# Performance work log

Measured on AMD Instinct MI355X. Metric: run time of the kernel, lower is better.

The kernel has to match this reference:

```python
import jax, jax.numpy as jnp
import numpy as np

N_NODES = 100_000
N_EDGES = 3_200_000
D_IN = 128
D_OUT = 128


def setup_inputs() -> dict:
    key = jax.random.key(0)
    k1, k2, k3, k4 = jax.random.split(key, 4)
    x = jax.random.normal(k1, (N_NODES, D_IN), dtype=jnp.float32)
    edge_index = jax.random.randint(k2, (2, N_EDGES), 0, N_NODES, dtype=jnp.int32)
    # nn.Linear(in, out): W is [out, in], b is [out]
    W = jax.random.normal(k3, (D_OUT, D_IN), dtype=jnp.float32) * (1.0 / np.sqrt(D_IN))
    b = jax.random.normal(k4, (D_OUT,), dtype=jnp.float32) * 0.01
    return {"x": x, "edge_index": edge_index, "W": W, "b": b}


def reference(x, edge_index, W, b):
    row, col = edge_index[0], edge_index[1]
    # deg = bincount(row); symmetric-normalization coefficients per edge
    deg = jax.ops.segment_sum(jnp.ones(row.shape[0], dtype=x.dtype), row,
                              num_segments=N_NODES)
    deg_inv_sqrt = jnp.where(deg > 0, jax.lax.rsqrt(deg), 0.0)
    norm = deg_inv_sqrt[row] * deg_inv_sqrt[col]  # [E]
    # linear transform then SpMM aggregation: out[i] = sum_{e: row[e]=i} norm[e] * xl[col[e]]
    xl = x @ W.T + b  # [N, D_OUT]
    out = jax.ops.segment_sum(norm[:, None] * xl[col], row, num_segments=N_NODES)
    return out
```

## Files before the change

### kernel.cpp

```cpp
#include <hip/hip_runtime.h>
#include <hip/hip_bf16.h>

#define N_NODES 100000
#define N_EDGES 3200000
#define D 128
#define NB 782
#define CAP 5120
#define EPB 32
#define K2 20

typedef __attribute__((ext_vector_type(8))) short short8v;
typedef __attribute__((ext_vector_type(4))) float f32x4;

static __device__ __forceinline__ short f2bf(float f) {
    __hip_bfloat16 h = __float2bfloat16(f);
    return __builtin_bit_cast(short, h);
}

__global__ __launch_bounds__(256) void partition_k(const int* __restrict__ ei,
                                                   int* __restrict__ cursor,
                                                   int* __restrict__ staging) {
    __shared__ int lbin[NB];
    int tid = threadIdx.x;
    long long base = (long long)blockIdx.x * (256 * EPB);

    for (int i = tid; i < NB; i += 256) lbin[i] = 0;
    __syncthreads();

    int lrec[EPB];
    int lpk[EPB];
#pragma unroll
    for (int j = 0; j < EPB; ++j) {
        long long e = base + j * 256 + tid;
        lpk[j] = -1;
        if (e < N_EDGES) {
            int r = ei[e];
            int c = ei[N_EDGES + e];
            int bin = r >> 7;
            int rank = atomicAdd(&lbin[bin], 1);
            lrec[j] = (c << 7) | (r & 127);
            lpk[j] = (bin << 16) | rank;
        }
    }
    __syncthreads();
    for (int i = tid; i < NB; i += 256) {
        int c = lbin[i];
        if (c > 0) lbin[i] = i * CAP + atomicAdd(&cursor[i], c);
    }
    __syncthreads();
#pragma unroll
    for (int j = 0; j < EPB; ++j) {
        if (lpk[j] >= 0) {
            int bin = ((unsigned)lpk[j]) >> 16;
            int rank = lpk[j] & 0xffff;
            staging[lbin[bin] + rank] = lrec[j];
        }
    }
}

__global__ __launch_bounds__(64) void bscan_k(const int* __restrict__ cursor,
                                              int* __restrict__ fbase) {
    int lane = threadIdx.x;
    const int CH = (NB + 63) / 64;
    int v[CH];
    int t = 0;
#pragma unroll
    for (int k = 0; k < CH; ++k) {
        int idx = lane * CH + k;
        int c = (idx < NB) ? cursor[idx] : 0;
        v[k] = t;
        t += c;
    }
    int x = t;
    for (int off = 1; off < 64; off <<= 1) {
        int y = __shfl_up(x, off, 64);
        if (lane >= off) x += y;
    }
    int excl = x - t;
#pragma unroll
    for (int k = 0; k < CH; ++k) {
        int idx = lane * CH + k;
        if (idx < NB) fbase[idx] = excl + v[k];
    }
}

__global__ __launch_bounds__(256) void pass2_k(const int* __restrict__ staging,
                                               const int* __restrict__ cursor,
                                               const int* __restrict__ fbase,
                                               int* __restrict__ rowptr,
                                               float* __restrict__ dinv,
                                               int* __restrict__ edgesF) {
    __shared__ int hist[128];
    __shared__ int ssc[128];
    int bin = blockIdx.x;
    int tid = threadIdx.x;
    int cnt = cursor[bin];
    int fb = fbase[bin];
    int row0 = bin << 7;
    const int* st = staging + bin * CAP;

    if (tid < 128) hist[tid] = 0;
    __syncthreads();

    int myrec[K2];
    int myrank[K2];
#pragma unroll
    for (int k = 0; k < K2; ++k) {
        int idx = k * 256 + tid;
        myrec[k] = (idx < cnt) ? st[idx] : -1;
    }
#pragma unroll
    for (int k = 0; k < K2; ++k) {
        myrank[k] = (myrec[k] >= 0) ? atomicAdd(&hist[myrec[k] & 127], 1) : 0;
    }
    __syncthreads();
    if (tid < 128) ssc[tid] = hist[tid];
    __syncthreads();
    for (int off = 1; off < 128; off <<= 1) {
        int t = (tid < 128 && tid >= off) ? ssc[tid - off] : 0;
        __syncthreads();
        if (tid < 128) ssc[tid] += t;
        __syncthreads();
    }
    if (tid < 128) {
        int row = row0 + tid;
        if (row < N_NODES) {
            int deg = hist[tid];
            rowptr[row] = fb + ssc[tid] - deg;
            dinv[row] = (deg > 0) ? rsqrtf((float)deg) : 0.0f;
        }
    }
    if (bin == 0 && tid == 0) rowptr[N_NODES] = N_EDGES;
    __syncthreads();
#pragma unroll
    for (int k = 0; k < K2; ++k) {
        if (myrec[k] >= 0) {
            int r = myrec[k] & 127;
            int c = ((unsigned)myrec[k]) >> 7;
            edgesF[fb + ssc[r] - hist[r] + myrank[k]] = c;
        }
    }
}

__global__ __launch_bounds__(256) void convW(const float* __restrict__ W,
                                             __hip_bfloat16* __restrict__ Wb) {
    int i = blockIdx.x * 256 + threadIdx.x;
    if (i < D * D) Wb[i] = __float2bfloat16(W[i]);
}

__global__ __launch_bounds__(256) void gemm_mfma(const float* __restrict__ x,
                                                 const __hip_bfloat16* __restrict__ Wb,
                                                 const float* __restrict__ b,
                                                 const float* __restrict__ dinv,
                                                 __hip_bfloat16* __restrict__ xl) {
    __shared__ __hip_bfloat16 lds[4][16][136];
    int tid = threadIdx.x;
    int w = tid >> 6;
    int l = tid & 63;
    int lm = l & 15;
    int kb = l >> 4;
    int bm = blockIdx.x * 64 + w * 16;

    int row = bm + lm;
    if (row >= N_NODES) row = N_NODES - 1;
    const float* xr = x + (size_t)row * D;

    short8v a[4];
#pragma unroll
    for (int ks = 0; ks < 4; ++ks) {
        const float* p = xr + ks * 32 + kb * 8;
        float4 u = *(const float4*)p;
        float4 v = *(const float4*)(p + 4);
        short8v t;
        t[0] = f2bf(u.x); t[1] = f2bf(u.y); t[2] = f2bf(u.z); t[3] = f2bf(u.w);
        t[4] = f2bf(v.x); t[5] = f2bf(v.y); t[6] = f2bf(v.z); t[7] = f2bf(v.w);
        a[ks] = t;
    }

    f32x4 acc[8];
#pragma unroll
    for (int nf = 0; nf < 8; ++nf) {
        acc[nf][0] = 0.f; acc[nf][1] = 0.f; acc[nf][2] = 0.f; acc[nf][3] = 0.f;
    }

    const short8v* Wv = reinterpret_cast<const short8v*>(Wb);
#pragma unroll
    for (int ks = 0; ks < 4; ++ks) {
#pragma unroll
        for (int nf = 0; nf < 8; ++nf) {
            short8v bf = Wv[(nf * 16 + lm) * 16 + ks * 4 + kb];
            acc[nf] = __builtin_amdgcn_mfma_f32_16x16x32_bf16(a[ks], bf, acc[nf], 0, 0, 0);
        }
    }

    float drj[4];
#pragma unroll
    for (int j = 0; j < 4; ++j) {
        int rr = bm + kb * 4 + j;
        if (rr >= N_NODES) rr = N_NODES - 1;
        drj[j] = dinv[rr];
    }

#pragma unroll
    for (int nf = 0; nf < 8; ++nf) {
        float bias = b[nf * 16 + lm];
#pragma unroll
        for (int j = 0; j < 4; ++j) {
            lds[w][kb * 4 + j][nf * 16 + lm] =
                __float2bfloat16((acc[nf][j] + bias) * drj[j]);
        }
    }
    __syncthreads();
#pragma unroll
    for (int it = 0; it < 4; ++it) {
        int idx = it * 64 + l;
        int r = idx >> 4;
        int ch = (idx & 15) * 8;
        int grow = bm + r;
        if (grow < N_NODES)
            *(short8v*)&xl[(size_t)grow * D + ch] = *(const short8v*)&lds[w][r][ch];
    }
}

__global__ __launch_bounds__(256) void aggregate(const int* __restrict__ edges,
                                                 const int* __restrict__ rowptr,
                                                 const float* __restrict__ dinv,
                                                 const __hip_bfloat16* __restrict__ xl,
                                                 float* __restrict__ out) {
    int gw = (blockIdx.x * 256 + threadIdx.x) >> 6;
    int lane = threadIdx.x & 63;
    if (gw >= N_NODES) return;
    int g = lane >> 4;
    int q = lane & 15;
    int s = rowptr[gw];
    int e = rowptr[gw + 1];

    float acc[8];
#pragma unroll
    for (int k = 0; k < 8; ++k) acc[k] = 0.0f;

    int i = s;
    for (; i + 4 <= e; i += 4) {
        int c = edges[i + g];
        uint4 v = *(const uint4*)&xl[(size_t)c * D + q * 8];
        acc[0] += __uint_as_float(v.x << 16);
        acc[1] += __uint_as_float(v.x & 0xffff0000u);
        acc[2] += __uint_as_float(v.y << 16);
        acc[3] += __uint_as_float(v.y & 0xffff0000u);
        acc[4] += __uint_as_float(v.z << 16);
        acc[5] += __uint_as_float(v.z & 0xffff0000u);
        acc[6] += __uint_as_float(v.w << 16);
        acc[7] += __uint_as_float(v.w & 0xffff0000u);
    }
    int rem = e - i;
    if (g < rem) {
        int c = edges[i + g];
        uint4 v = *(const uint4*)&xl[(size_t)c * D + q * 8];
        acc[0] += __uint_as_float(v.x << 16);
        acc[1] += __uint_as_float(v.x & 0xffff0000u);
        acc[2] += __uint_as_float(v.y << 16);
        acc[3] += __uint_as_float(v.y & 0xffff0000u);
        acc[4] += __uint_as_float(v.z << 16);
        acc[5] += __uint_as_float(v.z & 0xffff0000u);
        acc[6] += __uint_as_float(v.w << 16);
        acc[7] += __uint_as_float(v.w & 0xffff0000u);
    }
#pragma unroll
    for (int k = 0; k < 8; ++k) {
        acc[k] += __shfl_xor(acc[k], 16, 64);
        acc[k] += __shfl_xor(acc[k], 32, 64);
    }
    if (lane < 16) {
        float dr = dinv[gw];
        float4 o0 = make_float4(dr * acc[0], dr * acc[1], dr * acc[2], dr * acc[3]);
        float4 o1 = make_float4(dr * acc[4], dr * acc[5], dr * acc[6], dr * acc[7]);
        float* op = &out[(size_t)gw * D + q * 8];
        *(float4*)op = o0;
        *(float4*)(op + 4) = o1;
    }
}

extern "C" void kernel_launch(void* const* d_in, const int* in_sizes, int n_in,
                              void* d_out, int out_size, void* d_ws, size_t ws_size,
                              hipStream_t stream) {
    const float* x  = (const float*)d_in[0];
    const int*   ei = (const int*)d_in[1];
    const float* W  = (const float*)d_in[2];
    const float* b  = (const float*)d_in[3];
    float* out = (float*)d_out;

    unsigned int* ws = (unsigned int*)d_ws;
    __hip_bfloat16* xl = (__hip_bfloat16*)ws;
    __hip_bfloat16* Wb = (__hip_bfloat16*)(ws + 6400000);
    float* dinv    = (float*)(ws + 6408192);
    int*   rowptr  = (int*)(ws + 6508288);
    int*   cursor  = (int*)(ws + 6608448);
    int*   fbase   = (int*)(ws + 6609248);
    int*   edgesF  = (int*)(ws + 6610048);
    int*   staging = (int*)(ws + 9810048);

    hipMemsetAsync(cursor, 0, NB * sizeof(int), stream);

    const int pblocks = (N_EDGES + 256 * EPB - 1) / (256 * EPB);
    partition_k<<<pblocks, 256, 0, stream>>>(ei, cursor, staging);

    bscan_k<<<1, 64, 0, stream>>>(cursor, fbase);

    pass2_k<<<NB, 256, 0, stream>>>(staging, cursor, fbase, rowptr, dinv, edgesF);

    convW<<<(D * D + 255) / 256, 256, 0, stream>>>(W, Wb);

    gemm_mfma<<<(N_NODES + 63) / 64, 256, 0, stream>>>(x, Wb, b, dinv, xl);

    aggregate<<<(N_NODES * 64 + 255) / 256, 256, 0, stream>>>(
        edgesF, rowptr, dinv, xl, out);
}
```

Before: 318.8 us.

## Merge memset, W conversion and bin scan into fewer launches; unroll aggregate gather

```diff
diff --git a/kernel.cpp b/kernel.cpp
--- a/kernel.cpp
+++ b/kernel.cpp
@@ -15,6 +15,14 @@
 static __device__ __forceinline__ short f2bf(float f) {
     __hip_bfloat16 h = __float2bfloat16(f);
     return __builtin_bit_cast(short, h);
+}
+
+__global__ __launch_bounds__(256) void convW_init(const float* __restrict__ W,
+                                                  __hip_bfloat16* __restrict__ Wb,
+                                                  int* __restrict__ cursor) {
+    int i = blockIdx.x * 256 + threadIdx.x;
+    if (i < D * D) Wb[i] = __float2bfloat16(W[i]);
+    if (i < NB) cursor[i] = 0;
 }
 
 __global__ __launch_bounds__(256) void partition_k(const int* __restrict__ ei,
@@ -58,49 +66,28 @@
     }
 }
 
-__global__ __launch_bounds__(64) void bscan_k(const int* __restrict__ cursor,
-                                              int* __restrict__ fbase) {
-    int lane = threadIdx.x;
-    const int CH = (NB + 63) / 64;
-    int v[CH];
-    int t = 0;
-#pragma unroll
-    for (int k = 0; k < CH; ++k) {
-        int idx = lane * CH + k;
-        int c = (idx < NB) ? cursor[idx] : 0;
-        v[k] = t;
-        t += c;
-    }
-    int x = t;
-    for (int off = 1; off < 64; off <<= 1) {
-        int y = __shfl_up(x, off, 64);
-        if (lane >= off) x += y;
-    }
-    int excl = x - t;
-#pragma unroll
-    for (int k = 0; k < CH; ++k) {
-        int idx = lane * CH + k;
-        if (idx < NB) fbase[idx] = excl + v[k];
-    }
-}
-
 __global__ __launch_bounds__(256) void pass2_k(const int* __restrict__ staging,
                                                const int* __restrict__ cursor,
-                                               const int* __restrict__ fbase,
                                                int* __restrict__ rowptr,
                                                float* __restrict__ dinv,
                                                int* __restrict__ edgesF) {
     __shared__ int hist[128];
     __shared__ int ssc[128];
+    __shared__ int wsum[4];
     int bin = blockIdx.x;
     int tid = threadIdx.x;
     int cnt = cursor[bin];
-    int fb = fbase[bin];
     int row0 = bin << 7;
     const int* st = staging + bin * CAP;
 
+    int pacc = 0;
+    for (int j = tid; j < bin; j += 256) pacc += cursor[j];
+#pragma unroll
+    for (int off = 32; off > 0; off >>= 1) pacc += __shfl_down(pacc, off, 64);
+    if ((tid & 63) == 0) wsum[tid >> 6] = pacc;
     if (tid < 128) hist[tid] = 0;
     __syncthreads();
+    int fb = wsum[0] + wsum[1] + wsum[2] + wsum[3];
 
     int myrec[K2];
     int myrank[K2];
@@ -140,12 +127,6 @@
             edgesF[fb + ssc[r] - hist[r] + myrank[k]] = c;
         }
     }
-}
-
-__global__ __launch_bounds__(256) void convW(const float* __restrict__ W,
-                                             __hip_bfloat16* __restrict__ Wb) {
-    int i = blockIdx.x * 256 + threadIdx.x;
-    if (i < D * D) Wb[i] = __float2bfloat16(W[i]);
 }
 
 __global__ __launch_bounds__(256) void gemm_mfma(const float* __restrict__ x,
@@ -222,6 +203,17 @@
     }
 }
 
+static __device__ __forceinline__ void acc8(float* acc, uint4 v) {
+    acc[0] += __uint_as_float(v.x << 16);
+    acc[1] += __uint_as_float(v.x & 0xffff0000u);
+    acc[2] += __uint_as_float(v.y << 16);
+    acc[3] += __uint_as_float(v.y & 0xffff0000u);
+    acc[4] += __uint_as_float(v.z << 16);
+    acc[5] += __uint_as_float(v.z & 0xffff0000u);
+    acc[6] += __uint_as_float(v.w << 16);
+    acc[7] += __uint_as_float(v.w & 0xffff0000u);
+}
+
 __global__ __launch_bounds__(256) void aggregate(const int* __restrict__ edges,
                                                  const int* __restrict__ rowptr,
                                                  const float* __restrict__ dinv,
@@ -240,30 +232,27 @@
     for (int k = 0; k < 8; ++k) acc[k] = 0.0f;
 
     int i = s;
+    for (; i + 16 <= e; i += 16) {
+        int c0 = edges[i + g];
+        int c1 = edges[i + 4 + g];
+        int c2 = edges[i + 8 + g];
+        int c3 = edges[i + 12 + g];
+        uint4 v0 = *(const uint4*)&xl[(size_t)c0 * D + q * 8];
+        uint4 v1 = *(const uint4*)&xl[(size_t)c1 * D + q * 8];
+        uint4 v2 = *(const uint4*)&xl[(size_t)c2 * D + q * 8];
+        uint4 v3 = *(const uint4*)&xl[(size_t)c3 * D + q * 8];
+        acc8(acc, v0); acc8(acc, v1); acc8(acc, v2); acc8(acc, v3);
+    }
     for (; i + 4 <= e; i += 4) {
         int c = edges[i + g];
         uint4 v = *(const uint4*)&xl[(size_t)c * D + q * 8];
-        acc[0] += __uint_as_float(v.x << 16);
-        acc[1] += __uint_as_float(v.x & 0xffff0000u);
-        acc[2] += __uint_as_float(v.y << 16);
-        acc[3] += __uint_as_float(v.y & 0xffff0000u);
-        acc[4] += __uint_as_float(v.z << 16);
-        acc[5] += __uint_as_float(v.z & 0xffff0000u);
-        acc[6] += __uint_as_float(v.w << 16);
-        acc[7] += __uint_as_float(v.w & 0xffff0000u);
+        acc8(acc, v);
     }
     int rem = e - i;
     if (g < rem) {
         int c = edges[i + g];
         uint4 v = *(const uint4*)&xl[(size_t)c * D + q * 8];
-        acc[0] += __uint_as_float(v.x << 16);
-        acc[1] += __uint_as_float(v.x & 0xffff0000u);
-        acc[2] += __uint_as_float(v.y << 16);
-        acc[3] += __uint_as_float(v.y & 0xffff0000u);
-        acc[4] += __uint_as_float(v.z << 16);
-        acc[5] += __uint_as_float(v.z & 0xffff0000u);
-        acc[6] += __uint_as_float(v.w << 16);
-        acc[7] += __uint_as_float(v.w & 0xffff0000u);
+        acc8(acc, v);
     }
 #pragma unroll
     for (int k = 0; k < 8; ++k) {
@@ -295,20 +284,15 @@
     float* dinv    = (float*)(ws + 6408192);
     int*   rowptr  = (int*)(ws + 6508288);
     int*   cursor  = (int*)(ws + 6608448);
-    int*   fbase   = (int*)(ws + 6609248);
     int*   edgesF  = (int*)(ws + 6610048);
     int*   staging = (int*)(ws + 9810048);
 
-    hipMemsetAsync(cursor, 0, NB * sizeof(int), stream);
+    convW_init<<<(D * D + 255) / 256, 256, 0, stream>>>(W, Wb, cursor);
 
     const int pblocks = (N_EDGES + 256 * EPB - 1) / (256 * EPB);
     partition_k<<<pblocks, 256, 0, stream>>>(ei, cursor, staging);
 
-    bscan_k<<<1, 64, 0, stream>>>(cursor, fbase);
-
-    pass2_k<<<NB, 256, 0, stream>>>(staging, cursor, fbase, rowptr, dinv, edgesF);
-
-    convW<<<(D * D + 255) / 256, 256, 0, stream>>>(W, Wb);
+    pass2_k<<<NB, 256, 0, stream>>>(staging, cursor, rowptr, dinv, edgesF);
 
     gemm_mfma<<<(N_NODES + 63) / 64, 256, 0, stream>>>(x, Wb, b, dinv, xl);
 
```

Result: faster. 300.5 us (-5.7%).
